# Kernel optimization log

Measured on AMD Instinct MI355X. Metric: run time of the kernel, lower is better.

## Reference

```python
import jax, jax.numpy as jnp
import numpy as np


def setup_inputs() -> dict:
    key = jax.random.key(0)
    k1, k2, k3, k4 = jax.random.split(key, 4)
    B, T, C, H = 8, 2048, 1024, 1024
    return {
        "x": jax.random.normal(k1, (B, T, C), dtype=jnp.float32),
        "Wk": jax.random.normal(k2, (H, C), dtype=jnp.float32),
        "Wq": jax.random.normal(k3, (H, C), dtype=jnp.float32),
        "Wv": jax.random.normal(k4, (H, C), dtype=jnp.float32),
    }


def reference(x, Wk, Wq, Wv):
    # x: [B, T, C]; Wk/Wq/Wv: [H, C] (torch Linear stores [fan_out, fan_in])
    B, T, C = x.shape
    k = jnp.einsum('btc,hc->bth', x, Wk)  # [B, T, H]
    q = jnp.einsum('btc,hc->bth', x, Wq)
    v = jnp.einsum('btc,hc->bth', x, Wv)
    # NOTE: source scales by n_embd (C) ** -0.5, not head_size
    wei = jnp.einsum('bth,bsh->bts', q, k) * (C ** -0.5)  # [B, T, T]
    causal = jnp.tril(jnp.ones((T, T), dtype=bool))
    wei = jnp.where(causal, wei, -jnp.inf)
    wei = jax.nn.softmax(wei, axis=-1)
    # Dropout omitted (inference behavior; p=0.5 train-only in source)
    out = jnp.einsum('bts,bsh->bth', wei, v)  # [B, T, H]
    return (out, wei)
```

## Files before the change

### kernel.cpp

```cpp
#include <hip/hip_runtime.h>
#include <hip/hip_bf16.h>


#define BB 8
#define TT 2048
#define CC 1024
#define HH 1024
#define BT (BB * TT)

typedef _Float16 f16x8 __attribute__((ext_vector_type(8)));
typedef _Float16 f16x4 __attribute__((ext_vector_type(4)));
typedef float f32x4 __attribute__((ext_vector_type(4)));

#define AS1 __attribute__((address_space(1)))
#define AS3 __attribute__((address_space(3)))

__device__ __forceinline__ void gld16(const _Float16* g, _Float16* lds) {
    __builtin_amdgcn_global_load_lds((AS1 const unsigned int*)g,
                                     (AS3 unsigned int*)lds, 16, 0, 0);
}

__global__ __launch_bounds__(256) void split_kernel(
    const float* __restrict__ src, _Float16* __restrict__ dh,
    _Float16* __restrict__ dl, int n)
{
    int i = (blockIdx.x * 256 + threadIdx.x) * 4;
    if (i >= n) return;
    float4 v = *(const float4*)(src + i);
    f16x4 h, l;
    h[0] = (_Float16)v.x; l[0] = (_Float16)(v.x - (float)h[0]);
    h[1] = (_Float16)v.y; l[1] = (_Float16)(v.y - (float)h[1]);
    h[2] = (_Float16)v.z; l[2] = (_Float16)(v.z - (float)h[2]);
    h[3] = (_Float16)v.w; l[3] = (_Float16)(v.w - (float)h[3]);
    *(f16x4*)&dh[i] = h;
    *(f16x4*)&dl[i] = l;
}

__global__ __launch_bounds__(256) void splitT_kernel(
    const float* __restrict__ W, _Float16* __restrict__ th,
    _Float16* __restrict__ tl)
{
    __shared__ float L[64][65];
    const int h0 = blockIdx.x * 64;
    const int c0 = blockIdx.y * 64;
    const int tid = threadIdx.x;
    {
        const int hl = tid >> 2;
        const int cs = (tid & 3) * 16;
#pragma unroll
        for (int jj = 0; jj < 16; jj += 4) {
            float4 v = *(const float4*)&W[(size_t)(h0 + hl) * CC + c0 + cs + jj];
            L[cs + jj + 0][hl] = v.x;
            L[cs + jj + 1][hl] = v.y;
            L[cs + jj + 2][hl] = v.z;
            L[cs + jj + 3][hl] = v.w;
        }
    }
    __syncthreads();
    const int c  = tid >> 2;
    const int hs = (tid & 3) * 16;
    f16x8 hv0, hv1, lv0, lv1;
#pragma unroll
    for (int i = 0; i < 8; ++i) {
        float a = L[c][hs + i], b = L[c][hs + 8 + i];
        hv0[i] = (_Float16)a; lv0[i] = (_Float16)(a - (float)hv0[i]);
        hv1[i] = (_Float16)b; lv1[i] = (_Float16)(b - (float)hv1[i]);
    }
    size_t o = (size_t)(c0 + c) * HH + h0 + hs;
    *(f16x8*)&th[o] = hv0; *(f16x8*)&th[o + 8] = hv1;
    *(f16x8*)&tl[o] = lv0; *(f16x8*)&tl[o + 8] = lv1;
}

__global__ __launch_bounds__(256, 2) void mm_kernel(
    const _Float16* __restrict__ aH, const _Float16* __restrict__ aL,
    const _Float16* __restrict__ bH, const _Float16* __restrict__ bL,
    _Float16* __restrict__ mtH, _Float16* __restrict__ mtL)
{
    __shared__ _Float16 Ah[4096], Al[4096], Bh[4096], Bl[4096];

    const int n0 = blockIdx.x * 128;
    const int m0 = blockIdx.y * 128;

    const int tid  = threadIdx.x;
    const int r0   = tid & 127;
    const int k0   = tid >> 7;
    const int wave = tid >> 6;
    const int lane = tid & 63;
    const int quad = lane >> 4;
    const int lrow = lane & 15;
    const int wr   = (wave >> 1) * 64;
    const int wc   = (wave & 1) * 64;

    const size_t ga = (size_t)(m0 + r0) * HH + k0 * 8;
    const size_t gb = (size_t)(n0 + r0) * HH + k0 * 8;
    const int lds0 = tid * 8, lds1 = (tid + 256) * 8;

    f32x4 acc[4][4] = {};

    for (int kc = 0; kc < HH; kc += 32) {
        __syncthreads();
        gld16(aH + ga + kc,      &Ah[lds0]);
        gld16(aH + ga + kc + 16, &Ah[lds1]);
        gld16(aL + ga + kc,      &Al[lds0]);
        gld16(aL + ga + kc + 16, &Al[lds1]);
        gld16(bH + gb + kc,      &Bh[lds0]);
        gld16(bH + gb + kc + 16, &Bh[lds1]);
        gld16(bL + gb + kc,      &Bl[lds0]);
        gld16(bL + gb + kc + 16, &Bl[lds1]);
        __syncthreads();

        f16x8 ahf[4], alf[4], bhf[4], blf[4];
#pragma unroll
        for (int i = 0; i < 4; ++i) {
            ahf[i] = *(const f16x8*)&Ah[(quad * 128 + wr + i * 16 + lrow) * 8];
            alf[i] = *(const f16x8*)&Al[(quad * 128 + wr + i * 16 + lrow) * 8];
            bhf[i] = *(const f16x8*)&Bh[(quad * 128 + wc + i * 16 + lrow) * 8];
            blf[i] = *(const f16x8*)&Bl[(quad * 128 + wc + i * 16 + lrow) * 8];
        }
#pragma unroll
        for (int i = 0; i < 4; ++i)
#pragma unroll
            for (int j = 0; j < 4; ++j) {
                acc[i][j] = __builtin_amdgcn_mfma_f32_16x16x32_f16(ahf[i], bhf[j], acc[i][j], 0, 0, 0);
                acc[i][j] = __builtin_amdgcn_mfma_f32_16x16x32_f16(ahf[i], blf[j], acc[i][j], 0, 0, 0);
                acc[i][j] = __builtin_amdgcn_mfma_f32_16x16x32_f16(alf[i], bhf[j], acc[i][j], 0, 0, 0);
            }
    }

#pragma unroll
    for (int i = 0; i < 4; ++i)
#pragma unroll
        for (int j = 0; j < 4; ++j) {
            int mm = m0 + wr + i * 16 + quad * 4;
            int nn = n0 + wc + j * 16 + lrow;
            f16x4 ph, pl;
#pragma unroll
            for (int r = 0; r < 4; ++r) {
                float val = acc[i][j][r];
                _Float16 h = (_Float16)val;
                ph[r] = h;
                pl[r] = (_Float16)(val - (float)h);
            }
            *(f16x4*)&mtH[(size_t)nn * CC + mm] = ph;
            *(f16x4*)&mtL[(size_t)nn * CC + mm] = pl;
        }
}

#define EPI_STRIDE 136
__global__ __launch_bounds__(256, 2) void pv_kernel(
    const _Float16* __restrict__ xh, const _Float16* __restrict__ xl,
    const _Float16* __restrict__ mtH, const _Float16* __restrict__ mtL,
    const _Float16* __restrict__ Wvh,
    _Float16* __restrict__ Ph, _Float16* __restrict__ Pl,
    _Float16* __restrict__ vT)
{
    __shared__ _Float16 S[40960];

    const int idx   = blockIdx.x;
    const int z     = idx >> 10;
    const int r     = idx & 1023;
    const int xcd   = r & 7;
    const int j7    = r >> 3;
    const int mtile = xcd * 16 + (j7 >> 3);
    const int ntile = j7 & 7;
    const int m0 = mtile * 128;
    const int n0 = ntile * 128;

    const int tid  = threadIdx.x;
    const int r0   = tid & 127;
    const int k0   = tid >> 7;
    const int wave = tid >> 6;
    const int lane = tid & 63;
    const int quad = lane >> 4;
    const int lrow = lane & 15;
    const int wr   = (wave >> 1) * 64;
    const int wc   = (wave & 1) * 64;

    const size_t ga = (size_t)(m0 + r0) * CC + k0 * 8;
    const size_t gb = (size_t)(n0 + r0) * CC + k0 * 8;
    const int lds0 = tid * 8, lds1 = (tid + 256) * 8;

    f32x4 acc[4][4] = {};

    if (z == 0) {
#define PV_A(kc_, sp_) do { \
        _Float16* Sb = S + (sp_) * 8192; \
        gld16(xh + ga + (kc_),      &Sb[lds0]); \
        gld16(xh + ga + (kc_) + 16, &Sb[lds1]); \
        gld16(xl + ga + (kc_),      &Sb[4096 + lds0]); \
        gld16(xl + ga + (kc_) + 16, &Sb[4096 + lds1]); \
    } while (0)
#define PV_B(kc_, sp_) do { \
        _Float16* Sb = S + 24576 + (sp_) * 8192; \
        gld16(mtH + gb + (kc_),      &Sb[lds0]); \
        gld16(mtH + gb + (kc_) + 16, &Sb[lds1]); \
        gld16(mtL + gb + (kc_),      &Sb[4096 + lds0]); \
        gld16(mtL + gb + (kc_) + 16, &Sb[4096 + lds1]); \
    } while (0)
        PV_A(0, 0);
        PV_B(0, 0);
        PV_A(32, 1);
        int sa = 0, sb = 0;
        for (int kc = 0; kc < CC; kc += 32) {
            asm volatile("s_waitcnt vmcnt(4)" ::: "memory");
            __builtin_amdgcn_s_barrier();
            __builtin_amdgcn_sched_barrier(0);

            int kb = kc + 32; if (kb > CC - 32) kb = CC - 32;
            PV_B(kb, sb ^ 1);
            int ka = kc + 64; if (ka > CC - 32) ka = CC - 32;
            int s2 = sa + 2; if (s2 >= 3) s2 -= 3;
            PV_A(ka, s2);

            const _Float16* Ah = S + sa * 8192;
            const _Float16* Al = Ah + 4096;
            const _Float16* Bh = S + 24576 + sb * 8192;
            const _Float16* Bl = Bh + 4096;

            f16x8 ahf[4], alf[4], bhf[4], blf[4];
#pragma unroll
            for (int i = 0; i < 4; ++i) {
                ahf[i] = *(const f16x8*)&Ah[(quad * 128 + wr + i * 16 + lrow) * 8];
                alf[i] = *(const f16x8*)&Al[(quad * 128 + wr + i * 16 + lrow) * 8];
                bhf[i] = *(const f16x8*)&Bh[(quad * 128 + wc + i * 16 + lrow) * 8];
                blf[i] = *(const f16x8*)&Bl[(quad * 128 + wc + i * 16 + lrow) * 8];
            }
            __builtin_amdgcn_s_setprio(1);
#pragma unroll
            for (int i = 0; i < 4; ++i)
#pragma unroll
                for (int j = 0; j < 4; ++j) {
                    acc[i][j] = __builtin_amdgcn_mfma_f32_16x16x32_f16(ahf[i], bhf[j], acc[i][j], 0, 0, 0);
                    acc[i][j] = __builtin_amdgcn_mfma_f32_16x16x32_f16(ahf[i], blf[j], acc[i][j], 0, 0, 0);
                    acc[i][j] = __builtin_amdgcn_mfma_f32_16x16x32_f16(alf[i], bhf[j], acc[i][j], 0, 0, 0);
                }
            __builtin_amdgcn_s_setprio(0);

            ++sa; if (sa == 3) sa = 0;
            sb ^= 1;
        }
    } else {
#define PV_S1(kc_, sp_) do { \
        _Float16* Sb = S + (sp_) * 8192; \
        gld16(xh  + ga + (kc_),      &Sb[lds0]); \
        gld16(xh  + ga + (kc_) + 16, &Sb[lds1]); \
        gld16(Wvh + gb + (kc_),      &Sb[4096 + lds0]); \
        gld16(Wvh + gb + (kc_) + 16, &Sb[4096 + lds1]); \
    } while (0)
        PV_S1(0, 0);
        PV_S1(32, 1);
        int sl = 0;
        for (int kc = 0; kc < CC; kc += 32) {
            asm volatile("s_waitcnt vmcnt(4)" ::: "memory");
            __builtin_amdgcn_s_barrier();
            __builtin_amdgcn_sched_barrier(0);

            int kpre = kc + 64;
            if (kpre > CC - 32) kpre = CC - 32;
            int s2 = sl + 2; if (s2 >= 3) s2 -= 3;
            PV_S1(kpre, s2);

            const _Float16* Ah = S + sl * 8192;
            const _Float16* Bh = Ah + 4096;

            f16x8 ahf[4], bhf[4];
#pragma unroll
            for (int i = 0; i < 4; ++i) {
                ahf[i] = *(const f16x8*)&Ah[(quad * 128 + wr + i * 16 + lrow) * 8];
                bhf[i] = *(const f16x8*)&Bh[(quad * 128 + wc + i * 16 + lrow) * 8];
            }
            __builtin_amdgcn_s_setprio(1);
#pragma unroll
            for (int i = 0; i < 4; ++i)
#pragma unroll
                for (int j = 0; j < 4; ++j)
                    acc[i][j] = __builtin_amdgcn_mfma_f32_16x16x32_f16(ahf[i], bhf[j], acc[i][j], 0, 0, 0);
            __builtin_amdgcn_s_setprio(0);

            ++sl; if (sl == 3) sl = 0;
        }
    }

    asm volatile("s_waitcnt vmcnt(0)" ::: "memory");
    __syncthreads();

    if (z == 1) {
#pragma unroll
        for (int i = 0; i < 4; ++i)
#pragma unroll
            for (int j = 0; j < 4; ++j) {
                int hl = wc + j * 16 + lrow;
                int tl = wr + i * 16 + quad * 4;
                f16x4 p;
#pragma unroll
                for (int rr = 0; rr < 4; ++rr) p[rr] = (_Float16)acc[i][j][rr];
                *(f16x4*)&S[hl * EPI_STRIDE + tl] = p;
            }
        __syncthreads();
        const int bi  = mtile >> 4;
        const int t0g = (mtile & 15) * 128;
        _Float16* vb = vT + (size_t)bi * HH * TT;
#pragma unroll
        for (int rr = 0; rr < 128; rr += 16) {
            int h = rr + (tid >> 4);
            int t = (tid & 15) * 8;
            f16x8 val = *(const f16x8*)&S[h * EPI_STRIDE + t];
            *(f16x8*)&vb[(size_t)(n0 + h) * TT + t0g + t] = val;
        }
    } else {
#pragma unroll
        for (int i = 0; i < 4; ++i)
#pragma unroll
            for (int j = 0; j < 4; ++j) {
                int tl = wr + i * 16 + quad * 4;
                int cl = wc + j * 16 + lrow;
#pragma unroll
                for (int rr = 0; rr < 4; ++rr)
                    S[(tl + rr) * EPI_STRIDE + cl] = (_Float16)acc[i][j][rr];
            }
        __syncthreads();
#pragma unroll
        for (int rr = 0; rr < 128; rr += 16) {
            int t = rr + (tid >> 4);
            int c = (tid & 15) * 8;
            f16x8 val = *(const f16x8*)&S[t * EPI_STRIDE + c];
            *(f16x8*)&Ph[(size_t)(m0 + t) * CC + n0 + c] = val;
        }
        __syncthreads();
#pragma unroll
        for (int i = 0; i < 4; ++i)
#pragma unroll
            for (int j = 0; j < 4; ++j) {
                int tl = wr + i * 16 + quad * 4;
                int cl = wc + j * 16 + lrow;
#pragma unroll
                for (int rr = 0; rr < 4; ++rr) {
                    float val = acc[i][j][rr];
                    _Float16 h = (_Float16)val;
                    S[(tl + rr) * EPI_STRIDE + cl] = (_Float16)(val - (float)h);
                }
            }
        __syncthreads();
#pragma unroll
        for (int rr = 0; rr < 128; rr += 16) {
            int t = rr + (tid >> 4);
            int c = (tid & 15) * 8;
            f16x8 val = *(const f16x8*)&S[t * EPI_STRIDE + c];
            *(f16x8*)&Pl[(size_t)(m0 + t) * CC + n0 + c] = val;
        }
    }
}

__global__ __launch_bounds__(256, 2) void logits_kernel(
    const _Float16* __restrict__ Ph, const _Float16* __restrict__ Pl,
    const _Float16* __restrict__ xh, const _Float16* __restrict__ xl,
    float* __restrict__ wei)
{
    __shared__ _Float16 S[40960];

    const int id  = blockIdx.x;
    const int b   = id & 7;
    const int tri = id >> 3;
    int tt = (int)((sqrtf(8.0f * (float)tri + 1.0f) - 1.0f) * 0.5f);
    while ((tt + 1) * (tt + 2) / 2 <= tri) ++tt;
    while (tt * (tt + 1) / 2 > tri) --tt;
    const int st = tri - tt * (tt + 1) / 2;

    const size_t base = (size_t)b * TT * CC;
    float* wb = wei + (size_t)b * TT * TT;
    const int m0 = tt * 128;
    const int n0 = st * 128;

    const int tid  = threadIdx.x;
    const int r0   = tid & 127;
    const int k0   = tid >> 7;
    const int wave = tid >> 6;
    const int lane = tid & 63;
    const int quad = lane >> 4;
    const int lrow = lane & 15;
    const int wr   = (wave >> 1) * 64;
    const int wc   = (wave & 1) * 64;

    const size_t ga = base + (size_t)(m0 + r0) * CC + k0 * 8;
    const size_t gb = base + (size_t)(n0 + r0) * CC + k0 * 8;
    const int lds0 = tid * 8, lds1 = (tid + 256) * 8;

    f32x4 acc[4][4] = {};

#define LG_A(kc_, sp_) do { \
    _Float16* Sb = S + (sp_) * 8192; \
    gld16(Ph + ga + (kc_),      &Sb[lds0]); \
    gld16(Ph + ga + (kc_) + 16, &Sb[lds1]); \
    gld16(Pl + ga + (kc_),      &Sb[4096 + lds0]); \
    gld16(Pl + ga + (kc_) + 16, &Sb[4096 + lds1]); \
} while (0)
#define LG_B(kc_, sp_) do { \
    _Float16* Sb = S + 24576 + (sp_) * 8192; \
    gld16(xh + gb + (kc_),      &Sb[lds0]); \
    gld16(xh + gb + (kc_) + 16, &Sb[lds1]); \
    gld16(xl + gb + (kc_),      &Sb[4096 + lds0]); \
    gld16(xl + gb + (kc_) + 16, &Sb[4096 + lds1]); \
} while (0)

    LG_A(0, 0);
    LG_B(0, 0);
    LG_A(32, 1);

    int sa = 0, sb = 0;
    for (int kc = 0; kc < CC; kc += 32) {
        asm volatile("s_waitcnt vmcnt(4)" ::: "memory");
        __builtin_amdgcn_s_barrier();
        __builtin_amdgcn_sched_barrier(0);

        int kb = kc + 32; if (kb > CC - 32) kb = CC - 32;
        LG_B(kb, sb ^ 1);
        int ka = kc + 64; if (ka > CC - 32) ka = CC - 32;
        int s2 = sa + 2; if (s2 >= 3) s2 -= 3;
        LG_A(ka, s2);

        const _Float16* Ah = S + sa * 8192;
        const _Float16* Al = Ah + 4096;
        const _Float16* Bh = S + 24576 + sb * 8192;
        const _Float16* Bl = Bh + 4096;

        f16x8 ahf[4], alf[4], bhf[4], blf[4];
#pragma unroll
        for (int i = 0; i < 4; ++i) {
            ahf[i] = *(const f16x8*)&Ah[(quad * 128 + wr + i * 16 + lrow) * 8];
            alf[i] = *(const f16x8*)&Al[(quad * 128 + wr + i * 16 + lrow) * 8];
            bhf[i] = *(const f16x8*)&Bh[(quad * 128 + wc + i * 16 + lrow) * 8];
            blf[i] = *(const f16x8*)&Bl[(quad * 128 + wc + i * 16 + lrow) * 8];
        }
        __builtin_amdgcn_s_setprio(1);
#pragma unroll
        for (int i = 0; i < 4; ++i)
#pragma unroll
            for (int j = 0; j < 4; ++j) {
                acc[i][j] = __builtin_amdgcn_mfma_f32_16x16x32_f16(ahf[i], bhf[j], acc[i][j], 0, 0, 0);
                acc[i][j] = __builtin_amdgcn_mfma_f32_16x16x32_f16(ahf[i], blf[j], acc[i][j], 0, 0, 0);
                acc[i][j] = __builtin_amdgcn_mfma_f32_16x16x32_f16(alf[i], bhf[j], acc[i][j], 0, 0, 0);
            }
        __builtin_amdgcn_s_setprio(0);

        ++sa; if (sa == 3) sa = 0;
        sb ^= 1;
    }

    asm volatile("s_waitcnt vmcnt(0)" ::: "memory");

    const float scale = 0.03125f;
#pragma unroll
    for (int i = 0; i < 4; ++i)
#pragma unroll
        for (int j = 0; j < 4; ++j)
#pragma unroll
            for (int r = 0; r < 4; ++r) {
                int rr = wr + i * 16 + quad * 4 + r;
                int cc = wc + j * 16 + lrow;
                wb[(size_t)(m0 + rr) * TT + n0 + cc] = acc[i][j][r] * scale;
            }
}

__global__ __launch_bounds__(256) void softmax_kernel(
    float* __restrict__ wei, _Float16* __restrict__ wei16)
{
    const int t = blockIdx.x;
    const int b = blockIdx.y;
    float* row = wei + (size_t)b * TT * TT + (size_t)t * TT;
    _Float16* row16 = wei16 + (size_t)b * TT * TT + (size_t)t * TT;
    const int n = t + 1;
    const int tid = threadIdx.x;
    const int base = tid * 8;

    float vals[8];
    if (base < n) {
        float4 v0 = *(const float4*)&row[base];
        float4 v1 = *(const float4*)&row[base + 4];
        vals[0] = v0.x; vals[1] = v0.y; vals[2] = v0.z; vals[3] = v0.w;
        vals[4] = v1.x; vals[5] = v1.y; vals[6] = v1.z; vals[7] = v1.w;
    } else {
#pragma unroll
        for (int i = 0; i < 8; ++i) vals[i] = -INFINITY;
    }

    float mx = -INFINITY;
#pragma unroll
    for (int i = 0; i < 8; ++i) {
        if (base + i >= n) vals[i] = -INFINITY;
        mx = fmaxf(mx, vals[i]);
    }
#pragma unroll
    for (int off = 32; off > 0; off >>= 1)
        mx = fmaxf(mx, __shfl_down(mx, off));

    __shared__ float redm[4];
    __shared__ float reds[4];
    if ((tid & 63) == 0) redm[tid >> 6] = mx;
    __syncthreads();
    const float m = fmaxf(fmaxf(redm[0], redm[1]), fmaxf(redm[2], redm[3]));

    float sum = 0.f;
#pragma unroll
    for (int i = 0; i < 8; ++i) {
        vals[i] = __expf(vals[i] - m);
        sum += vals[i];
    }
#pragma unroll
    for (int off = 32; off > 0; off >>= 1)
        sum += __shfl_down(sum, off);
    if ((tid & 63) == 0) reds[tid >> 6] = sum;
    __syncthreads();
    const float inv = 1.0f / (reds[0] + reds[1] + reds[2] + reds[3]);

    f16x8 h;
#pragma unroll
    for (int i = 0; i < 8; ++i) {
        float w = vals[i] * inv;
        vals[i] = w;
        h[i] = (_Float16)w;
    }
    *(float4*)&row[base]     = make_float4(vals[0], vals[1], vals[2], vals[3]);
    *(float4*)&row[base + 4] = make_float4(vals[4], vals[5], vals[6], vals[7]);
    *(f16x8*)&row16[base]    = h;
}

__global__ __launch_bounds__(256, 3) void out_kernel(
    const _Float16* __restrict__ wei16, const _Float16* __restrict__ vT,
    float* __restrict__ out)
{
    __shared__ _Float16 S[24576];

    const int id = blockIdx.x;
    const int b  = id & 7;
    const int r  = id >> 3;
    const int tt = 15 - (r >> 3);
    const int nb = r & 7;

    const _Float16* wb = wei16 + (size_t)b * TT * TT;
    const _Float16* vb = vT    + (size_t)b * HH * TT;
    float*          ob = out   + (size_t)b * TT * HH;

    const int m0 = tt * 128;
    const int n0 = nb * 128;
    const int kend = (tt + 1) * 128;

    const int tid  = threadIdx.x;
    const int r0   = tid & 127;
    const int k0   = tid >> 7;
    const int wave = tid >> 6;
    const int lane = tid & 63;
    const int quad = lane >> 4;
    const int lrow = lane & 15;
    const int wr   = (wave >> 1) * 64;
    const int wc   = (wave & 1) * 64;

    const size_t ga = (size_t)(m0 + r0) * TT + k0 * 8;
    const size_t gb = (size_t)(n0 + r0) * TT + k0 * 8;
    const int lds0 = tid * 8, lds1 = (tid + 256) * 8;

    f32x4 acc[4][4] = {};

#define OUT_STAGE(kc_, sp_) do { \
    _Float16* Sb = S + (sp_) * 8192; \
    gld16(wb + ga + (kc_),      &Sb[lds0]); \
    gld16(wb + ga + (kc_) + 16, &Sb[lds1]); \
    gld16(vb + gb + (kc_),      &Sb[4096 + lds0]); \
    gld16(vb + gb + (kc_) + 16, &Sb[4096 + lds1]); \
} while (0)

    OUT_STAGE(0, 0);
    OUT_STAGE(32, 1);

    int sl = 0;
    for (int kc = 0; kc < kend; kc += 32) {
        asm volatile("s_waitcnt vmcnt(4)" ::: "memory");
        __builtin_amdgcn_s_barrier();
        __builtin_amdgcn_sched_barrier(0);

        int kpre = kc + 64;
        if (kpre > kend - 32) kpre = kend - 32;
        int s2 = sl + 2; if (s2 >= 3) s2 -= 3;
        OUT_STAGE(kpre, s2);

        const _Float16* Ah = S + sl * 8192;
        const _Float16* Bh = Ah + 4096;

        f16x8 ahf[4], bhf[4];
#pragma unroll
        for (int i = 0; i < 4; ++i) {
            ahf[i] = *(const f16x8*)&Ah[(quad * 128 + wr + i * 16 + lrow) * 8];
            bhf[i] = *(const f16x8*)&Bh[(quad * 128 + wc + i * 16 + lrow) * 8];
        }
        __builtin_amdgcn_s_setprio(1);
#pragma unroll
        for (int i = 0; i < 4; ++i)
#pragma unroll
            for (int j = 0; j < 4; ++j)
                acc[i][j] = __builtin_amdgcn_mfma_f32_16x16x32_f16(ahf[i], bhf[j], acc[i][j], 0, 0, 0);
        __builtin_amdgcn_s_setprio(0);

        ++sl; if (sl == 3) sl = 0;
    }

    asm volatile("s_waitcnt vmcnt(0)" ::: "memory");

#pragma unroll
    for (int i = 0; i < 4; ++i)
#pragma unroll
        for (int j = 0; j < 4; ++j)
#pragma unroll
            for (int r2 = 0; r2 < 4; ++r2) {
                int rr = wr + i * 16 + quad * 4 + r2;
                int cc = wc + j * 16 + lrow;
                ob[(size_t)(m0 + rr) * HH + n0 + cc] = acc[i][j][r2];
            }
}

extern "C" void kernel_launch(void* const* d_in, const int* in_sizes, int n_in,
                              void* d_out, int out_size, void* d_ws, size_t ws_size,
                              hipStream_t stream)
{
    const float* x  = (const float*)d_in[0];
    const float* Wk = (const float*)d_in[1];
    const float* Wq = (const float*)d_in[2];
    const float* Wv = (const float*)d_in[3];

    const size_t NX = (size_t)BT * CC;
    const size_t NW = (size_t)HH * CC;

    float* out = (float*)d_out;
    float* wei = out + (size_t)BT * HH;

    _Float16* WqTh = (_Float16*)out;
    _Float16* WqTl = WqTh + NW;
    _Float16* WkTh = WqTl + NW;
    _Float16* WkTl = WkTh + NW;
    _Float16* Wvh  = WkTl + NW;
    _Float16* Wvl  = Wvh  + NW;
    _Float16* MTh  = Wvl  + NW;
    _Float16* MTl  = MTh  + NW;

    _Float16* xh = (_Float16*)d_ws;
    _Float16* xl = xh + NX;
    _Float16* Ph = xl + NX;
    _Float16* Pl = Ph + NX;
    _Float16* vT = Pl + NX;
    _Float16* wei16 = (_Float16*)d_ws;

    split_kernel<<<dim3(NX / 1024), 256, 0, stream>>>(x, xh, xl, (int)NX);
    splitT_kernel<<<dim3(HH / 64, CC / 64), 256, 0, stream>>>(Wq, WqTh, WqTl);
    splitT_kernel<<<dim3(HH / 64, CC / 64), 256, 0, stream>>>(Wk, WkTh, WkTl);
    split_kernel<<<dim3(NW / 1024), 256, 0, stream>>>(Wv, Wvh, Wvl, (int)NW);

    mm_kernel<<<dim3(CC / 128, CC / 128), 256, 0, stream>>>(
        WqTh, WqTl, WkTh, WkTl, MTh, MTl);
    pv_kernel<<<dim3(2048), 256, 0, stream>>>(
        xh, xl, MTh, MTl, Wvh, Ph, Pl, vT);
    logits_kernel<<<dim3(136 * BB), 256, 0, stream>>>(
        Ph, Pl, xh, xl, wei);
    softmax_kernel<<<dim3(TT, BB), 256, 0, stream>>>(wei, wei16);
    out_kernel<<<dim3(128 * BB), 256, 0, stream>>>(wei16, vT, out);
}
```

Before: 800.8 us.

## Load B operand fragments directly from global into registers, bypassing LDS

In the pv, logits and out GEMM kernels, the B-side operand is no longer staged through LDS with global_load_lds double buffering. Each wave now reads its B fragments straight from global memory into registers at the start of each k-step. Only the A tile stays in LDS, which shrinks the shared-memory footprint and removes the LDS write/read traffic for B. In exchange, global latency for B is exposed inside each iteration because there is no prefetch. B data is also fetched redundantly by the waves that share a column block, which adds L2/global traffic.

```diff
diff --git a/kernel.cpp b/kernel.cpp
--- a/kernel.cpp
+++ b/kernel.cpp
@@ -154,7 +154,7 @@
     _Float16* __restrict__ Ph, _Float16* __restrict__ Pl,
     _Float16* __restrict__ vT)
 {
-    __shared__ _Float16 S[40960];
+    __shared__ _Float16 S[24576];
 
     const int idx   = blockIdx.x;
     const int z     = idx >> 10;
@@ -177,7 +177,6 @@
     const int wc   = (wave & 1) * 64;
 
     const size_t ga = (size_t)(m0 + r0) * CC + k0 * 8;
-    const size_t gb = (size_t)(n0 + r0) * CC + k0 * 8;
     const int lds0 = tid * 8, lds1 = (tid + 256) * 8;
 
     f32x4 acc[4][4] = {};
@@ -190,40 +189,35 @@
         gld16(xl + ga + (kc_),      &Sb[4096 + lds0]); \
         gld16(xl + ga + (kc_) + 16, &Sb[4096 + lds1]); \
     } while (0)
-#define PV_B(kc_, sp_) do { \
-        _Float16* Sb = S + 24576 + (sp_) * 8192; \
-        gld16(mtH + gb + (kc_),      &Sb[lds0]); \
-        gld16(mtH + gb + (kc_) + 16, &Sb[lds1]); \
-        gld16(mtL + gb + (kc_),      &Sb[4096 + lds0]); \
-        gld16(mtL + gb + (kc_) + 16, &Sb[4096 + lds1]); \
-    } while (0)
         PV_A(0, 0);
-        PV_B(0, 0);
         PV_A(32, 1);
-        int sa = 0, sb = 0;
+        int sa = 0;
         for (int kc = 0; kc < CC; kc += 32) {
             asm volatile("s_waitcnt vmcnt(4)" ::: "memory");
             __builtin_amdgcn_s_barrier();
             __builtin_amdgcn_sched_barrier(0);
 
-            int kb = kc + 32; if (kb > CC - 32) kb = CC - 32;
-            PV_B(kb, sb ^ 1);
+            f16x8 bhf[4], blf[4];
+#pragma unroll
+            for (int j = 0; j < 4; ++j) {
+                const size_t gbj = (size_t)(n0 + wc + j * 16 + lrow) * CC + kc + quad * 8;
+                bhf[j] = *(const f16x8*)&mtH[gbj];
+                blf[j] = *(const f16x8*)&mtL[gbj];
+            }
+            __builtin_amdgcn_sched_barrier(0);
+
             int ka = kc + 64; if (ka > CC - 32) ka = CC - 32;
             int s2 = sa + 2; if (s2 >= 3) s2 -= 3;
             PV_A(ka, s2);
+            __builtin_amdgcn_sched_barrier(0);
 
             const _Float16* Ah = S + sa * 8192;
             const _Float16* Al = Ah + 4096;
-            const _Float16* Bh = S + 24576 + sb * 8192;
-            const _Float16* Bl = Bh + 4096;
-
-            f16x8 ahf[4], alf[4], bhf[4], blf[4];
+            f16x8 ahf[4], alf[4];
 #pragma unroll
             for (int i = 0; i < 4; ++i) {
                 ahf[i] = *(const f16x8*)&Ah[(quad * 128 + wr + i * 16 + lrow) * 8];
                 alf[i] = *(const f16x8*)&Al[(quad * 128 + wr + i * 16 + lrow) * 8];
-                bhf[i] = *(const f16x8*)&Bh[(quad * 128 + wc + i * 16 + lrow) * 8];
-                blf[i] = *(const f16x8*)&Bl[(quad * 128 + wc + i * 16 + lrow) * 8];
             }
             __builtin_amdgcn_s_setprio(1);
 #pragma unroll
@@ -237,38 +231,39 @@
             __builtin_amdgcn_s_setprio(0);
 
             ++sa; if (sa == 3) sa = 0;
-            sb ^= 1;
         }
     } else {
 #define PV_S1(kc_, sp_) do { \
-        _Float16* Sb = S + (sp_) * 8192; \
-        gld16(xh  + ga + (kc_),      &Sb[lds0]); \
-        gld16(xh  + ga + (kc_) + 16, &Sb[lds1]); \
-        gld16(Wvh + gb + (kc_),      &Sb[4096 + lds0]); \
-        gld16(Wvh + gb + (kc_) + 16, &Sb[4096 + lds1]); \
+        _Float16* Sb = S + (sp_) * 4096; \
+        gld16(xh + ga + (kc_),      &Sb[lds0]); \
+        gld16(xh + ga + (kc_) + 16, &Sb[lds1]); \
     } while (0)
         PV_S1(0, 0);
         PV_S1(32, 1);
         int sl = 0;
         for (int kc = 0; kc < CC; kc += 32) {
-            asm volatile("s_waitcnt vmcnt(4)" ::: "memory");
+            asm volatile("s_waitcnt vmcnt(2)" ::: "memory");
             __builtin_amdgcn_s_barrier();
             __builtin_amdgcn_sched_barrier(0);
 
-            int kpre = kc + 64;
-            if (kpre > CC - 32) kpre = CC - 32;
+            f16x8 bhf[4];
+#pragma unroll
+            for (int j = 0; j < 4; ++j) {
+                const size_t gbj = (size_t)(n0 + wc + j * 16 + lrow) * CC + kc + quad * 8;
+                bhf[j] = *(const f16x8*)&Wvh[gbj];
+            }
+            __builtin_amdgcn_sched_barrier(0);
+
+            int ka = kc + 64; if (ka > CC - 32) ka = CC - 32;
             int s2 = sl + 2; if (s2 >= 3) s2 -= 3;
-            PV_S1(kpre, s2);
-
-            const _Float16* Ah = S + sl * 8192;
-            const _Float16* Bh = Ah + 4096;
-
-            f16x8 ahf[4], bhf[4];
-#pragma unroll
-            for (int i = 0; i < 4; ++i) {
+            PV_S1(ka, s2);
+            __builtin_amdgcn_sched_barrier(0);
+
+            const _Float16* Ah = S + sl * 4096;
+            f16x8 ahf[4];
+#pragma unroll
+            for (int i = 0; i < 4; ++i)
                 ahf[i] = *(const f16x8*)&Ah[(quad * 128 + wr + i * 16 + lrow) * 8];
-                bhf[i] = *(const f16x8*)&Bh[(quad * 128 + wc + i * 16 + lrow) * 8];
-            }
             __builtin_amdgcn_s_setprio(1);
 #pragma unroll
             for (int i = 0; i < 4; ++i)
@@ -356,7 +351,7 @@
     const _Float16* __restrict__ xh, const _Float16* __restrict__ xl,
     float* __restrict__ wei)
 {
-    __shared__ _Float16 S[40960];
+    __shared__ _Float16 S[24576];
 
     const int id  = blockIdx.x;
     const int b   = id & 7;
@@ -382,7 +377,8 @@
     const int wc   = (wave & 1) * 64;
 
     const size_t ga = base + (size_t)(m0 + r0) * CC + k0 * 8;
-    const size_t gb = base + (size_t)(n0 + r0) * CC + k0 * 8;
+    const _Float16* xhb = xh + base;
+    const _Float16* xlb = xl + base;
     const int lds0 = tid * 8, lds1 = (tid + 256) * 8;
 
     f32x4 acc[4][4] = {};
@@ -394,42 +390,37 @@
     gld16(Pl + ga + (kc_),      &Sb[4096 + lds0]); \
     gld16(Pl + ga + (kc_) + 16, &Sb[4096 + lds1]); \
 } while (0)
-#define LG_B(kc_, sp_) do { \
-    _Float16* Sb = S + 24576 + (sp_) * 8192; \
-    gld16(xh + gb + (kc_),      &Sb[lds0]); \
-    gld16(xh + gb + (kc_) + 16, &Sb[lds1]); \
-    gld16(xl + gb + (kc_),      &Sb[4096 + lds0]); \
-    gld16(xl + gb + (kc_) + 16, &Sb[4096 + lds1]); \
-} while (0)
 
     LG_A(0, 0);
-    LG_B(0, 0);
     LG_A(32, 1);
 
-    int sa = 0, sb = 0;
+    int sa = 0;
     for (int kc = 0; kc < CC; kc += 32) {
         asm volatile("s_waitcnt vmcnt(4)" ::: "memory");
         __builtin_amdgcn_s_barrier();
         __builtin_amdgcn_sched_barrier(0);
 
-        int kb = kc + 32; if (kb > CC - 32) kb = CC - 32;
-        LG_B(kb, sb ^ 1);
+        f16x8 bhf[4], blf[4];
+#pragma unroll
+        for (int j = 0; j < 4; ++j) {
+            const size_t gbj = (size_t)(n0 + wc + j * 16 + lrow) * CC + kc + quad * 8;
+            bhf[j] = *(const f16x8*)&xhb[gbj];
+            blf[j] = *(const f16x8*)&xlb[gbj];
+        }
+        __builtin_amdgcn_sched_barrier(0);
+
         int ka = kc + 64; if (ka > CC - 32) ka = CC - 32;
         int s2 = sa + 2; if (s2 >= 3) s2 -= 3;
         LG_A(ka, s2);
+        __builtin_amdgcn_sched_barrier(0);
 
         const _Float16* Ah = S + sa * 8192;
         const _Float16* Al = Ah + 4096;
-        const _Float16* Bh = S + 24576 + sb * 8192;
-        const _Float16* Bl = Bh + 4096;
-
-        f16x8 ahf[4], alf[4], bhf[4], blf[4];
+        f16x8 ahf[4], alf[4];
 #pragma unroll
         for (int i = 0; i < 4; ++i) {
             ahf[i] = *(const f16x8*)&Ah[(quad * 128 + wr + i * 16 + lrow) * 8];
             alf[i] = *(const f16x8*)&Al[(quad * 128 + wr + i * 16 + lrow) * 8];
-            bhf[i] = *(const f16x8*)&Bh[(quad * 128 + wc + i * 16 + lrow) * 8];
-            blf[i] = *(const f16x8*)&Bl[(quad * 128 + wc + i * 16 + lrow) * 8];
         }
         __builtin_amdgcn_s_setprio(1);
 #pragma unroll
@@ -443,7 +434,6 @@
         __builtin_amdgcn_s_setprio(0);
 
         ++sa; if (sa == 3) sa = 0;
-        sb ^= 1;
     }
 
     asm volatile("s_waitcnt vmcnt(0)" ::: "memory");
@@ -528,7 +518,7 @@
     const _Float16* __restrict__ wei16, const _Float16* __restrict__ vT,
     float* __restrict__ out)
 {
-    __shared__ _Float16 S[24576];
+    __shared__ _Float16 S[12288];
 
     const int id = blockIdx.x;
     const int b  = id & 7;
@@ -555,42 +545,43 @@
     const int wc   = (wave & 1) * 64;
 
     const size_t ga = (size_t)(m0 + r0) * TT + k0 * 8;
-    const size_t gb = (size_t)(n0 + r0) * TT + k0 * 8;
     const int lds0 = tid * 8, lds1 = (tid + 256) * 8;
 
     f32x4 acc[4][4] = {};
 
-#define OUT_STAGE(kc_, sp_) do { \
-    _Float16* Sb = S + (sp_) * 8192; \
+#define OUT_A(kc_, sp_) do { \
+    _Float16* Sb = S + (sp_) * 4096; \
     gld16(wb + ga + (kc_),      &Sb[lds0]); \
     gld16(wb + ga + (kc_) + 16, &Sb[lds1]); \
-    gld16(vb + gb + (kc_),      &Sb[4096 + lds0]); \
-    gld16(vb + gb + (kc_) + 16, &Sb[4096 + lds1]); \
 } while (0)
 
-    OUT_STAGE(0, 0);
-    OUT_STAGE(32, 1);
+    OUT_A(0, 0);
+    OUT_A(32, 1);
 
     int sl = 0;
     for (int kc = 0; kc < kend; kc += 32) {
-        asm volatile("s_waitcnt vmcnt(4)" ::: "memory");
+        asm volatile("s_waitcnt vmcnt(2)" ::: "memory");
         __builtin_amdgcn_s_barrier();
         __builtin_amdgcn_sched_barrier(0);
 
-        int kpre = kc + 64;
-        if (kpre > kend - 32) kpre = kend - 32;
+        f16x8 bhf[4];
+#pragma unroll
+        for (int j = 0; j < 4; ++j) {
+            const size_t gbj = (size_t)(n0 + wc + j * 16 + lrow) * TT + kc + quad * 8;
+            bhf[j] = *(const f16x8*)&vb[gbj];
+        }
+        __builtin_amdgcn_sched_barrier(0);
+
+        int ka = kc + 64; if (ka > kend - 32) ka = kend - 32;
         int s2 = sl + 2; if (s2 >= 3) s2 -= 3;
-        OUT_STAGE(kpre, s2);
-
-        const _Float16* Ah = S + sl * 8192;
-        const _Float16* Bh = Ah + 4096;
-
-        f16x8 ahf[4], bhf[4];
-#pragma unroll
-        for (int i = 0; i < 4; ++i) {
+        OUT_A(ka, s2);
+        __builtin_amdgcn_sched_barrier(0);
+
+        const _Float16* Ah = S + sl * 4096;
+        f16x8 ahf[4];
+#pragma unroll
+        for (int i = 0; i < 4; ++i)
             ahf[i] = *(const f16x8*)&Ah[(quad * 128 + wr + i * 16 + lrow) * 8];
-            bhf[i] = *(const f16x8*)&Bh[(quad * 128 + wc + i * 16 + lrow) * 8];
-        }
         __builtin_amdgcn_s_setprio(1);
 #pragma unroll
         for (int i = 0; i < 4; ++i)
```

Result: slower. 967.3 us (+20.8%).
